# Performance work log

Hardware: AMD Instinct MI355X
Metric: run time of the kernel (lower is better)

## Reference

```python
import jax, jax.numpy as jnp
import numpy as np

N, E = 50000, 800000
NFEAT, NHID, NCLASS = 128, 64, 40
LN_EPS = 1e-5


def setup_inputs() -> dict:
    key = jax.random.key(0)
    ks = jax.random.split(key, 10)
    x = jax.random.normal(ks[0], (N, NFEAT), dtype=jnp.float32)
    edge_index = jax.random.randint(ks[1], (2, E), 0, N, dtype=jnp.int32)
    adj_vals = jax.random.uniform(ks[2], (E,), dtype=jnp.float32)
    s1 = 1.0 / NHID ** 0.5
    W1 = jax.random.uniform(ks[3], (NFEAT, NHID), minval=-s1, maxval=s1, dtype=jnp.float32)
    s2 = 1.0 / (2 * NHID) ** 0.5
    a1 = jax.random.uniform(ks[4], (2 * NHID, 1), minval=-s2, maxval=s2, dtype=jnp.float32)
    s3 = 1.0 / NCLASS ** 0.5
    W2 = jax.random.uniform(ks[5], (NHID, NCLASS), minval=-s3, maxval=s3, dtype=jnp.float32)
    # residual projection Linear(nfeat, nclass)
    sl = 1.0 / NFEAT ** 0.5
    res_w = jax.random.uniform(ks[6], (NCLASS, NFEAT), minval=-sl, maxval=sl, dtype=jnp.float32)
    res_b = jax.random.uniform(ks[7], (NCLASS,), minval=-sl, maxval=sl, dtype=jnp.float32)
    ln_g = jnp.ones((NCLASS,), dtype=jnp.float32)
    ln_b = jnp.zeros((NCLASS,), dtype=jnp.float32)
    return {"x": x, "edge_index": edge_index, "adj_vals": adj_vals,
            "W1": W1, "a1": a1, "W2": W2, "res_w": res_w, "res_b": res_b,
            "ln_g": ln_g, "ln_b": ln_b}


def reference(x, edge_index, adj_vals, W1, a1, W2, res_w, res_b, ln_g, ln_b):
    n = x.shape[0]
    row, col = edge_index[0], edge_index[1]
    h1 = x @ W1                                  # [N, nhid]
    # edge attention: cat([h1[row], h1[col]]) @ a1 == h1[row]@a_src + h1[col]@a_dst
    a_src, a_dst = a1[:NHID, 0], a1[NHID:, 0]
    scores = h1[row] @ a_src + h1[col] @ a_dst   # [E]
    scores = jax.nn.leaky_relu(scores, negative_slope=0.2)
    w = jax.nn.sigmoid(scores) * adj_vals        # [E] weighted adjacency values
    # sparse mm: out[row] += w * h[col]
    h1_out = jax.ops.segment_sum(w[:, None] * h1[col], row, num_segments=n)
    h1_out = jax.nn.relu(h1_out)
    h2 = h1_out @ W2                             # [N, nclass]
    h2_out = jax.ops.segment_sum(w[:, None] * h2[col], row, num_segments=n)
    h2_out = jax.nn.relu(h2_out)
    # residual projection + LayerNorm
    y = h2_out + (x @ res_w.T + res_b)
    mu = jnp.mean(y, axis=-1, keepdims=True)
    var = jnp.var(y, axis=-1, keepdims=True)
    y = (y - mu) * jax.lax.rsqrt(var + LN_EPS) * ln_g + ln_b
    return y
```

## Files before the change

### kernel.cpp

```cpp
#include <hip/hip_runtime.h>
#include <math.h>

#define N_NODES 50000
#define N_EDGES 800000
#define NFEAT 128
#define NHID 64
#define NCLASS 40
#define LN_EPS 1e-5f
#define BROWS 64
#define NBUCK ((N_NODES + BROWS - 1) / BROWS)
#define CHUNK 4096
#define NCHUNK ((N_EDGES + CHUNK - 1) / CHUNK)
#define NPB 16
#define H2ROWS 64

__device__ __forceinline__ int swz(int k) { return ((k >> 2) & 7) << 2; }

__device__ __forceinline__ unsigned packbf(float a, float b) {
  unsigned ua = __float_as_uint(a), ub = __float_as_uint(b);
  ua += 0x7fffu + ((ua >> 16) & 1u);
  ub += 0x7fffu + ((ub >> 16) & 1u);
  return (ua >> 16) | (ub & 0xffff0000u);
}
__device__ __forceinline__ unsigned bf16hi(float a) {
  unsigned u = __float_as_uint(a);
  u += 0x7fffu + ((u >> 16) & 1u);
  return u & 0xffff0000u;
}
__device__ __forceinline__ float lo16(unsigned v) { return __uint_as_float(v << 16); }
__device__ __forceinline__ float hi16(unsigned v) { return __uint_as_float(v & 0xffff0000u); }

__global__ __launch_bounds__(256) void k_h1mm(const float* __restrict__ x,
    const float* __restrict__ W1, const float* __restrict__ a1,
    unsigned* __restrict__ h1u, float* __restrict__ s_src, float* __restrict__ s_dst,
    int* __restrict__ bcnt) {
  __shared__ float xT[NFEAT * 64];
  __shared__ float W1s[NFEAT * NHID];
  int t = threadIdx.x;
  if (blockIdx.x == 0)
    for (int i = t; i < NBUCK; i += 256) bcnt[i] = 0;
  int R0 = blockIdx.x * 64;
  for (int i = t; i < NFEAT * NHID / 4; i += 256)
    ((float4*)W1s)[i] = ((const float4*)W1)[i];
#pragma unroll
  for (int it = 0; it < 8; ++it) {
    int i = t + it * 256;
    int r = i >> 5, kq = i & 31;
    int gr = R0 + r;
    float4 v = make_float4(0.f, 0.f, 0.f, 0.f);
    if (gr < N_NODES) v = *(const float4*)(x + (size_t)gr * NFEAT + kq * 4);
    int rw = r ^ ((kq & 7) << 2);
    xT[(kq * 4 + 0) * 64 + rw] = v.x;
    xT[(kq * 4 + 1) * 64 + rw] = v.y;
    xT[(kq * 4 + 2) * 64 + rw] = v.z;
    xT[(kq * 4 + 3) * 64 + rw] = v.w;
  }
  __syncthreads();
  int cg = t & 15, rg = t >> 4;
  int c0 = cg * 4, r0 = rg * 4;
  float acc[4][4] = {};
#pragma unroll 4
  for (int k = 0; k < NFEAT; ++k) {
    float4 xv = *(const float4*)&xT[k * 64 + (r0 ^ swz(k))];
    float4 wv = *(const float4*)&W1s[k * NHID + c0];
    float xr[4] = {xv.x, xv.y, xv.z, xv.w};
    float wr[4] = {wv.x, wv.y, wv.z, wv.w};
#pragma unroll
    for (int j = 0; j < 4; ++j)
#pragma unroll
      for (int c = 0; c < 4; ++c)
        acc[j][c] = fmaf(xr[j], wr[c], acc[j][c]);
  }
  float4 as = *(const float4*)(a1 + c0);
  float4 ad = *(const float4*)(a1 + NHID + c0);
  float asr[4] = {as.x, as.y, as.z, as.w};
  float adr[4] = {ad.x, ad.y, ad.z, ad.w};
  float ps[4], pd[4];
#pragma unroll
  for (int j = 0; j < 4; ++j) {
    int gr = R0 + r0 + j;
    if (gr < N_NODES) {
      uint2 pk;
      pk.x = packbf(acc[j][0], acc[j][1]);
      pk.y = packbf(acc[j][2], acc[j][3]);
      *(uint2*)&h1u[(size_t)gr * 32 + (c0 >> 1)] = pk;
    }
    float s = 0.f, d = 0.f;
#pragma unroll
    for (int c = 0; c < 4; ++c) {
      s = fmaf(acc[j][c], asr[c], s);
      d = fmaf(acc[j][c], adr[c], d);
    }
    ps[j] = s; pd[j] = d;
  }
#pragma unroll
  for (int j = 0; j < 4; ++j)
#pragma unroll
    for (int off = 1; off < 16; off <<= 1) {
      ps[j] += __shfl_xor(ps[j], off);
      pd[j] += __shfl_xor(pd[j], off);
    }
  if (cg == 0) {
#pragma unroll
    for (int j = 0; j < 4; ++j) {
      int gr = R0 + r0 + j;
      if (gr < N_NODES) { s_src[gr] = ps[j]; s_dst[gr] = pd[j]; }
    }
  }
}

__global__ __launch_bounds__(256) void k_resmm(const float* __restrict__ x,
    const float* __restrict__ res_w, const float* __restrict__ res_b,
    float* __restrict__ res) {
  __shared__ float xT[NFEAT * 128];
  __shared__ float rwT[NFEAT * NCLASS];
  int t = threadIdx.x;
  int R0 = blockIdx.x * 128;
  for (int i = t; i < NCLASS * NFEAT; i += 256) {
    int c = i / NFEAT, k = i % NFEAT;
    rwT[k * NCLASS + c] = res_w[i];
  }
#pragma unroll
  for (int it = 0; it < 16; ++it) {
    int i = t + it * 256;
    int r = i >> 5, kq = i & 31;
    int gr = R0 + r;
    float4 v = make_float4(0.f, 0.f, 0.f, 0.f);
    if (gr < N_NODES) v = *(const float4*)(x + (size_t)gr * NFEAT + kq * 4);
    int rw = r ^ ((kq & 7) << 2);
    xT[(kq * 4 + 0) * 128 + rw] = v.x;
    xT[(kq * 4 + 1) * 128 + rw] = v.y;
    xT[(kq * 4 + 2) * 128 + rw] = v.z;
    xT[(kq * 4 + 3) * 128 + rw] = v.w;
  }
  __syncthreads();
  int cg = t & 7, rg = t >> 3;
  int c0 = cg * 5, r0 = rg * 4;
  float acc[4][5] = {};
#pragma unroll 4
  for (int k = 0; k < NFEAT; ++k) {
    float4 xv = *(const float4*)&xT[k * 128 + (r0 ^ swz(k))];
    float xr[4] = {xv.x, xv.y, xv.z, xv.w};
    float wr[5];
#pragma unroll
    for (int c = 0; c < 5; ++c) wr[c] = rwT[k * NCLASS + c0 + c];
#pragma unroll
    for (int j = 0; j < 4; ++j)
#pragma unroll
      for (int c = 0; c < 5; ++c)
        acc[j][c] = fmaf(xr[j], wr[c], acc[j][c]);
  }
  float bb[5];
#pragma unroll
  for (int c = 0; c < 5; ++c) bb[c] = res_b[c0 + c];
#pragma unroll
  for (int j = 0; j < 4; ++j) {
    int gr = R0 + r0 + j;
    if (gr < N_NODES) {
#pragma unroll
      for (int c = 0; c < 5; ++c)
        res[(size_t)gr * NCLASS + c0 + c] = acc[j][c] + bb[c];
    }
  }
}

__global__ __launch_bounds__(256) void k_bhist(const int* __restrict__ ei,
    int* __restrict__ bcnt) {
  __shared__ int cnt[NBUCK];
  int t = threadIdx.x;
  int e0 = blockIdx.x * CHUNK;
  int ecnt = min(CHUNK, N_EDGES - e0);
  for (int i = t; i < NBUCK; i += 256) cnt[i] = 0;
  __syncthreads();
  for (int i = t; i < ecnt; i += 256)
    atomicAdd(&cnt[ei[e0 + i] >> 6], 1);
  __syncthreads();
  for (int i = t; i < NBUCK; i += 256)
    if (cnt[i]) atomicAdd(&bcnt[i], cnt[i]);
}

__global__ __launch_bounds__(256) void k_bscan(const int* __restrict__ bcnt,
    int* __restrict__ gptr, int* __restrict__ gfill) {
  __shared__ int psum[256];
  int t = threadIdx.x;
  int base = t * 4;
  int s[4];
#pragma unroll
  for (int j = 0; j < 4; ++j)
    s[j] = (base + j < NBUCK) ? bcnt[base + j] : 0;
  int local = s[0] + s[1] + s[2] + s[3];
  psum[t] = local;
  __syncthreads();
#pragma unroll
  for (int o = 1; o < 256; o <<= 1) {
    int v = (t >= o) ? psum[t - o] : 0;
    __syncthreads();
    psum[t] += v;
    __syncthreads();
  }
  int excl = psum[t] - local;
#pragma unroll
  for (int j = 0; j < 4; ++j) {
    if (base + j < NBUCK) gptr[base + j] = excl;
    excl += s[j];
  }
  if (t == 255) gptr[NBUCK] = psum[255];
  for (int i = t; i < NBUCK; i += 256) gfill[i] = 0;
}

__global__ __launch_bounds__(256) void k_bscatter(const int* __restrict__ ei,
    const float* __restrict__ adj, const int* __restrict__ gptr,
    int* __restrict__ gfill, uint2* __restrict__ edata) {
  __shared__ int cnt[NBUCK];
  __shared__ int off[NBUCK];
  __shared__ int gbase[NBUCK];
  __shared__ int po[NBUCK];
  __shared__ int psum[256];
  __shared__ uint2 stage[CHUNK];
  int t = threadIdx.x;
  int e0 = blockIdx.x * CHUNK;
  int ecnt = min(CHUNK, N_EDGES - e0);
  for (int i = t; i < NBUCK; i += 256) { cnt[i] = 0; po[i] = 0; }
  __syncthreads();
  for (int i = t; i < ecnt; i += 256)
    atomicAdd(&cnt[ei[e0 + i] >> 6], 1);
  __syncthreads();
  int base = t * 4;
  int s0 = (base < NBUCK) ? cnt[base] : 0;
  int s1 = (base + 1 < NBUCK) ? cnt[base + 1] : 0;
  int s2 = (base + 2 < NBUCK) ? cnt[base + 2] : 0;
  int s3 = (base + 3 < NBUCK) ? cnt[base + 3] : 0;
  int local = s0 + s1 + s2 + s3;
  psum[t] = local;
  __syncthreads();
#pragma unroll
  for (int o = 1; o < 256; o <<= 1) {
    int v = (t >= o) ? psum[t - o] : 0;
    __syncthreads();
    psum[t] += v;
    __syncthreads();
  }
  int excl = psum[t] - local;
  if (base < NBUCK) {
    off[base] = excl;
    if (s0 > 0) gbase[base] = gptr[base] + atomicAdd(&gfill[base], s0);
  }
  if (base + 1 < NBUCK) {
    off[base + 1] = excl + s0;
    if (s1 > 0) gbase[base + 1] = gptr[base + 1] + atomicAdd(&gfill[base + 1], s1);
  }
  if (base + 2 < NBUCK) {
    off[base + 2] = excl + s0 + s1;
    if (s2 > 0) gbase[base + 2] = gptr[base + 2] + atomicAdd(&gfill[base + 2], s2);
  }
  if (base + 3 < NBUCK) {
    off[base + 3] = excl + s0 + s1 + s2;
    if (s3 > 0) gbase[base + 3] = gptr[base + 3] + atomicAdd(&gfill[base + 3], s3);
  }
  __syncthreads();
  for (int i = t; i < ecnt; i += 256) {
    int e = e0 + i;
    int row = ei[e], col = ei[N_EDGES + e];
    int b = row >> 6;
    int pos = off[b] + atomicAdd(&po[b], 1);
    stage[pos] = make_uint2(((unsigned)b << 22) | ((unsigned)(row & 63) << 16) |
                            (unsigned)col, __float_as_uint(adj[e]));
  }
  __syncthreads();
  for (int i = t; i < ecnt; i += 256) {
    uint2 v = stage[i];
    int b = v.x >> 22;
    edata[(size_t)gbase[b] + (i - off[b])] = v;
  }
}

__global__ __launch_bounds__(256) void k_csr(const uint2* __restrict__ edata,
    const int* __restrict__ gptr, const float* __restrict__ s_src,
    const float* __restrict__ s_dst, int* __restrict__ row_ptr,
    unsigned* __restrict__ ecsr) {
  __shared__ int lcnt[BROWS];
  __shared__ int lexcl[BROWS];
  __shared__ int lfill[BROWS];
  __shared__ float ssrc[BROWS];
  int t = threadIdx.x;
  int b = blockIdx.x;
  int es = gptr[b], ee = gptr[b + 1];
  if (t < BROWS) {
    lcnt[t] = 0; lfill[t] = 0;
    int gn = b * BROWS + t;
    ssrc[t] = (gn < N_NODES) ? s_src[gn] : 0.f;
  }
  __syncthreads();
  for (int i = es + t; i < ee; i += 256)
    atomicAdd(&lcnt[(edata[i].x >> 16) & 63u], 1);
  __syncthreads();
  if (t < 64) {
    int v = lcnt[t];
    int sc = v;
#pragma unroll
    for (int o = 1; o < 64; o <<= 1) {
      int u = __shfl_up(sc, o);
      if (t >= o) sc += u;
    }
    lexcl[t] = sc - v;
    int gn = b * BROWS + t;
    if (gn < N_NODES) row_ptr[gn] = es + sc - v;
  }
  if (b == NBUCK - 1 && t == 0) row_ptr[N_NODES] = ee;
  __syncthreads();
  for (int i = es + t; i < ee; i += 256) {
    uint2 v = edata[i];
    int rl = (v.x >> 16) & 63;
    int col = v.x & 0xffffu;
    float sc = ssrc[rl] + s_dst[col];
    sc = (sc > 0.f) ? sc : 0.2f * sc;
    float wv = __uint_as_float(v.y) / (1.f + __expf(-sc));
    int pos = es + lexcl[rl] + atomicAdd(&lfill[rl], 1);
    ecsr[pos] = bf16hi(wv) | (unsigned)col;
  }
}

__global__ __launch_bounds__(256) void k_agg1(const unsigned* __restrict__ h1u,
    const unsigned* __restrict__ edata, const int* __restrict__ row_ptr,
    unsigned* __restrict__ h1o) {
  __shared__ int rps[NPB + 1];
  __shared__ float accs[NPB][NHID];
  int t = threadIdx.x;
  int n0 = blockIdx.x * NPB;
  if (t <= NPB) rps[t] = row_ptr[min(n0 + t, N_NODES)];
  for (int i = t; i < NPB * NHID / 4; i += 256)
    ((float4*)&accs[0][0])[i] = make_float4(0.f, 0.f, 0.f, 0.f);
  __syncthreads();
  int e0 = rps[0], e1 = rps[NPB];
  int span = e1 - e0;
  int gid = t >> 5, s = t & 31;
  int chunk = (span + 7) >> 3;
  int es = e0 + gid * chunk;
  int ee = min(es + chunk, e1);
  if (es < ee) {
    int lo = 0, hi = NPB - 1;
    while (lo < hi) { int mid = (lo + hi) >> 1; if (rps[mid + 1] <= es) lo = mid + 1; else hi = mid; }
    int r = lo, nxt = rps[r + 1];
    float acc0 = 0.f, acc1 = 0.f;
    int e = es;
    while (e < ee) {
      int m = ee - e; if (m > 8) m = 8;
      unsigned ue = (s < m) ? edata[e + s] : 0u;
      unsigned u[8], v[8];
#pragma unroll
      for (int i = 0; i < 8; ++i) u[i] = __shfl(ue, i, 32);
#pragma unroll
      for (int i = 0; i < 8; ++i) if (i < m) v[i] = h1u[(size_t)(u[i] & 0xffffu) * 32 + s];
#pragma unroll
      for (int i = 0; i < 8; ++i) if (i < m) {
        while (e + i >= nxt) {
          atomicAdd(&accs[r][2 * s], acc0);
          atomicAdd(&accs[r][2 * s + 1], acc1);
          acc0 = acc1 = 0.f; ++r; nxt = rps[r + 1];
        }
        float wv = hi16(u[i]);
        acc0 = fmaf(wv, lo16(v[i]), acc0);
        acc1 = fmaf(wv, hi16(v[i]), acc1);
      }
      e += m;
    }
    atomicAdd(&accs[r][2 * s], acc0);
    atomicAdd(&accs[r][2 * s + 1], acc1);
  }
  __syncthreads();
  for (int i = t; i < NPB * 32; i += 256) {
    int n = i >> 5, c = i & 31;
    int gn = n0 + n;
    if (gn < N_NODES)
      h1o[(size_t)gn * 32 + c] =
          packbf(fmaxf(accs[n][2 * c], 0.f), fmaxf(accs[n][2 * c + 1], 0.f));
  }
}

__global__ __launch_bounds__(256) void k_h2mm(const unsigned* __restrict__ h1o,
    const float* __restrict__ W2, unsigned short* __restrict__ h2s) {
  __shared__ unsigned xs[H2ROWS * 32];
  __shared__ float W2s[NHID * NCLASS];
  int t = threadIdx.x;
  int R0 = blockIdx.x * H2ROWS;
  for (int i = t; i < NHID * NCLASS; i += 256) W2s[i] = W2[i];
  for (int i = t; i < H2ROWS * 32; i += 256) {
    int r = i >> 5, ku = i & 31;
    int gr = R0 + r;
    unsigned v = (gr < N_NODES) ? h1o[(size_t)gr * 32 + ku] : 0u;
    xs[r * 32 + (ku ^ (r & 31))] = v;
  }
  __syncthreads();
  int q = t & 31, cg = t >> 5;
  int c0 = cg * 5;
  float acc[2][5] = {};
#pragma unroll 8
  for (int ku = 0; ku < 32; ++ku) {
    unsigned ua = xs[q * 32 + (ku ^ q)];
    unsigned ub = xs[(q + 32) * 32 + (ku ^ q)];
    float a0 = lo16(ua), a1 = hi16(ua);
    float b0 = lo16(ub), b1 = hi16(ub);
#pragma unroll
    for (int c = 0; c < 5; ++c) {
      float w0 = W2s[(2 * ku) * NCLASS + c0 + c];
      float w1 = W2s[(2 * ku + 1) * NCLASS + c0 + c];
      acc[0][c] = fmaf(a0, w0, acc[0][c]);
      acc[0][c] = fmaf(a1, w1, acc[0][c]);
      acc[1][c] = fmaf(b0, w0, acc[1][c]);
      acc[1][c] = fmaf(b1, w1, acc[1][c]);
    }
  }
#pragma unroll
  for (int j = 0; j < 2; ++j) {
    int gr = R0 + q + j * 32;
    if (gr < N_NODES) {
#pragma unroll
      for (int c = 0; c < 5; ++c)
        h2s[(size_t)gr * NCLASS + c0 + c] = (unsigned short)(bf16hi(acc[j][c]) >> 16);
    }
  }
}

__global__ __launch_bounds__(256) void k_agg2(const unsigned short* __restrict__ h2s,
    const unsigned* __restrict__ edata, const int* __restrict__ row_ptr,
    const float* __restrict__ res, const float* __restrict__ ln_g,
    const float* __restrict__ ln_b, float* __restrict__ out) {
  __shared__ int rps[NPB + 1];
  __shared__ float accs[NPB][NCLASS];
  int t = threadIdx.x;
  int n0 = blockIdx.x * NPB;
  if (t <= NPB) rps[t] = row_ptr[min(n0 + t, N_NODES)];
  for (int i = t; i < NPB * NCLASS; i += 256) ((float*)accs)[i] = 0.f;
  __syncthreads();
  int e0 = rps[0], e1 = rps[NPB];
  int span = e1 - e0;
  int gid = t >> 5, s = t & 31;
  int chunk = (span + 7) >> 3;
  int es = e0 + gid * chunk;
  int ee = min(es + chunk, e1);
  bool act = (s < 20);
  if (es < ee) {
    int lo = 0, hi = NPB - 1;
    while (lo < hi) { int mid = (lo + hi) >> 1; if (rps[mid + 1] <= es) lo = mid + 1; else hi = mid; }
    int r = lo, nxt = rps[r + 1];
    float acc0 = 0.f, acc1 = 0.f;
    int e = es;
    while (e < ee) {
      int m = ee - e; if (m > 8) m = 8;
      unsigned ue = (s < m) ? edata[e + s] : 0u;
      unsigned u[8], v[8];
#pragma unroll
      for (int i = 0; i < 8; ++i) u[i] = __shfl(ue, i, 32);
#pragma unroll
      for (int i = 0; i < 8; ++i) {
        v[i] = 0u;
        if (i < m && act)
          v[i] = *(const unsigned*)(h2s + (size_t)(u[i] & 0xffffu) * NCLASS + 2 * s);
      }
#pragma unroll
      for (int i = 0; i < 8; ++i) if (i < m) {
        while (e + i >= nxt) {
          if (act) {
            atomicAdd(&accs[r][2 * s], acc0);
            atomicAdd(&accs[r][2 * s + 1], acc1);
          }
          acc0 = acc1 = 0.f; ++r; nxt = rps[r + 1];
        }
        float wv = hi16(u[i]);
        acc0 = fmaf(wv, lo16(v[i]), acc0);
        acc1 = fmaf(wv, hi16(v[i]), acc1);
      }
      e += m;
    }
    if (act) {
      atomicAdd(&accs[r][2 * s], acc0);
      atomicAdd(&accs[r][2 * s + 1], acc1);
    }
  }
  __syncthreads();
  int wave = t >> 6, lane = t & 63;
  for (int k = 0; k < NPB / 4; ++k) {
    int n = wave * (NPB / 4) + k;
    int gn = n0 + n;
    if (gn >= N_NODES) break;
    float y = 0.f;
    if (lane < NCLASS)
      y = fmaxf(accs[n][lane], 0.f) + res[(size_t)gn * NCLASS + lane];
    float s1 = y, s2 = y * y;
#pragma unroll
    for (int off = 1; off < 64; off <<= 1) {
      s1 += __shfl_xor(s1, off);
      s2 += __shfl_xor(s2, off);
    }
    float mu = s1 / (float)NCLASS;
    float var = s2 / (float)NCLASS - mu * mu;
    float inv = rsqrtf(var + LN_EPS);
    if (lane < NCLASS)
      out[(size_t)gn * NCLASS + lane] = (y - mu) * inv * ln_g[lane] + ln_b[lane];
  }
}

extern "C" void kernel_launch(void* const* d_in, const int* in_sizes, int n_in,
                              void* d_out, int out_size, void* d_ws, size_t ws_size,
                              hipStream_t stream) {
  const float* x     = (const float*)d_in[0];
  const int*   ei    = (const int*)  d_in[1];
  const float* adj   = (const float*)d_in[2];
  const float* W1    = (const float*)d_in[3];
  const float* a1    = (const float*)d_in[4];
  const float* W2    = (const float*)d_in[5];
  const float* res_w = (const float*)d_in[6];
  const float* res_b = (const float*)d_in[7];
  const float* ln_g  = (const float*)d_in[8];
  const float* ln_b  = (const float*)d_in[9];
  float* out = (float*)d_out;

  char* ws = (char*)d_ws;
  size_t off = 0;
  auto alloc = [&](size_t bytes) -> void* {
    void* p = (void*)(ws + off);
    off += (bytes + 255) & ~(size_t)255;
    return p;
  };

  unsigned*       h1u     = (unsigned*)alloc((size_t)N_NODES * 32 * 4);
  float*          s_src   = (float*)alloc((size_t)N_NODES * 4);
  float*          s_dst   = (float*)alloc((size_t)N_NODES * 4);
  int*            bcnt    = (int*)alloc((size_t)NBUCK * 4);
  int*            gptr    = (int*)alloc((size_t)(NBUCK + 1) * 4);
  int*            gfill   = (int*)alloc((size_t)NBUCK * 4);
  int*            row_ptr = (int*)alloc((size_t)(N_NODES + 1) * 4);
  uint2*          edata   = (uint2*)alloc((size_t)N_EDGES * 8);
  unsigned*       ecsr    = (unsigned*)alloc((size_t)N_EDGES * 4);
  unsigned*       h1o     = (unsigned*)alloc((size_t)N_NODES * 32 * 4);
  unsigned short* h2s     = (unsigned short*)alloc((size_t)N_NODES * NCLASS * 2);
  float*          res     = (float*)alloc((size_t)N_NODES * NCLASS * 4);
  (void)ws_size; (void)in_sizes; (void)n_in; (void)out_size;

  const int NBLK_H1  = (N_NODES + 63) / 64;
  const int NBLK_RES = (N_NODES + 127) / 128;
  const int NBLK_H2  = (N_NODES + H2ROWS - 1) / H2ROWS;
  const int NBLK_AGG = (N_NODES + NPB - 1) / NPB;

  k_h1mm<<<NBLK_H1, 256, 0, stream>>>(x, W1, a1, h1u, s_src, s_dst, bcnt);
  k_resmm<<<NBLK_RES, 256, 0, stream>>>(x, res_w, res_b, res);
  k_bhist<<<NCHUNK, 256, 0, stream>>>(ei, bcnt);
  k_bscan<<<1, 256, 0, stream>>>(bcnt, gptr, gfill);
  k_bscatter<<<NCHUNK, 256, 0, stream>>>(ei, adj, gptr, gfill, edata);
  k_csr<<<NBUCK, 256, 0, stream>>>(edata, gptr, s_src, s_dst, row_ptr, ecsr);
  k_agg1<<<NBLK_AGG, 256, 0, stream>>>(h1u, ecsr, row_ptr, h1o);
  k_h2mm<<<NBLK_H2, 256, 0, stream>>>(h1o, W2, h2s);
  k_agg2<<<NBLK_AGG, 256, 0, stream>>>(h2s, ecsr, row_ptr, res, ln_g, ln_b, out);
}
```

Baseline: 191.7 us.

## Reorder second layer to aggregate h1 then apply W2 in agg2 epilogue

Uses linearity, (A·h1o)·W2 = A·(h1o·W2), to drop the separate h2 matmul kernel and its bf16 h2 buffer. The second aggregation now gathers 64-wide bf16 h1o rows (128 B) per edge instead of 40-wide h2 rows (80 B). Each block multiplies its 16 aggregated rows by W2, held in shared memory, before the LayerNorm epilogue. This saves one launch and an N×40 write and read, but raises gather traffic per edge and adds a W2 load per block. It also changes rounding, since h2 is no longer quantised to bf16.

```diff
diff --git a/kernel.cpp b/kernel.cpp
--- a/kernel.cpp
+++ b/kernel.cpp
@@ -12,7 +12,6 @@
 #define CHUNK 4096
 #define NCHUNK ((N_EDGES + CHUNK - 1) / CHUNK)
 #define NPB 16
-#define H2ROWS 64
 
 __device__ __forceinline__ int swz(int k) { return ((k >> 2) & 7) << 2; }
 
@@ -377,60 +376,20 @@
   }
 }
 
-__global__ __launch_bounds__(256) void k_h2mm(const unsigned* __restrict__ h1o,
-    const float* __restrict__ W2, unsigned short* __restrict__ h2s) {
-  __shared__ unsigned xs[H2ROWS * 32];
+__global__ __launch_bounds__(256) void k_agg2(const unsigned* __restrict__ h1o,
+    const unsigned* __restrict__ edata, const int* __restrict__ row_ptr,
+    const float* __restrict__ W2, const float* __restrict__ res,
+    const float* __restrict__ ln_g, const float* __restrict__ ln_b,
+    float* __restrict__ out) {
+  __shared__ int rps[NPB + 1];
+  __shared__ float accs[NPB][NHID];
   __shared__ float W2s[NHID * NCLASS];
-  int t = threadIdx.x;
-  int R0 = blockIdx.x * H2ROWS;
-  for (int i = t; i < NHID * NCLASS; i += 256) W2s[i] = W2[i];
-  for (int i = t; i < H2ROWS * 32; i += 256) {
-    int r = i >> 5, ku = i & 31;
-    int gr = R0 + r;
-    unsigned v = (gr < N_NODES) ? h1o[(size_t)gr * 32 + ku] : 0u;
-    xs[r * 32 + (ku ^ (r & 31))] = v;
-  }
-  __syncthreads();
-  int q = t & 31, cg = t >> 5;
-  int c0 = cg * 5;
-  float acc[2][5] = {};
-#pragma unroll 8
-  for (int ku = 0; ku < 32; ++ku) {
-    unsigned ua = xs[q * 32 + (ku ^ q)];
-    unsigned ub = xs[(q + 32) * 32 + (ku ^ q)];
-    float a0 = lo16(ua), a1 = hi16(ua);
-    float b0 = lo16(ub), b1 = hi16(ub);
-#pragma unroll
-    for (int c = 0; c < 5; ++c) {
-      float w0 = W2s[(2 * ku) * NCLASS + c0 + c];
-      float w1 = W2s[(2 * ku + 1) * NCLASS + c0 + c];
-      acc[0][c] = fmaf(a0, w0, acc[0][c]);
-      acc[0][c] = fmaf(a1, w1, acc[0][c]);
-      acc[1][c] = fmaf(b0, w0, acc[1][c]);
-      acc[1][c] = fmaf(b1, w1, acc[1][c]);
-    }
-  }
-#pragma unroll
-  for (int j = 0; j < 2; ++j) {
-    int gr = R0 + q + j * 32;
-    if (gr < N_NODES) {
-#pragma unroll
-      for (int c = 0; c < 5; ++c)
-        h2s[(size_t)gr * NCLASS + c0 + c] = (unsigned short)(bf16hi(acc[j][c]) >> 16);
-    }
-  }
-}
-
-__global__ __launch_bounds__(256) void k_agg2(const unsigned short* __restrict__ h2s,
-    const unsigned* __restrict__ edata, const int* __restrict__ row_ptr,
-    const float* __restrict__ res, const float* __restrict__ ln_g,
-    const float* __restrict__ ln_b, float* __restrict__ out) {
-  __shared__ int rps[NPB + 1];
-  __shared__ float accs[NPB][NCLASS];
   int t = threadIdx.x;
   int n0 = blockIdx.x * NPB;
   if (t <= NPB) rps[t] = row_ptr[min(n0 + t, N_NODES)];
-  for (int i = t; i < NPB * NCLASS; i += 256) ((float*)accs)[i] = 0.f;
+  for (int i = t; i < NHID * NCLASS; i += 256) W2s[i] = W2[i];
+  for (int i = t; i < NPB * NHID / 4; i += 256)
+    ((float4*)&accs[0][0])[i] = make_float4(0.f, 0.f, 0.f, 0.f);
   __syncthreads();
   int e0 = rps[0], e1 = rps[NPB];
   int span = e1 - e0;
@@ -438,7 +397,6 @@
   int chunk = (span + 7) >> 3;
   int es = e0 + gid * chunk;
   int ee = min(es + chunk, e1);
-  bool act = (s < 20);
   if (es < ee) {
     int lo = 0, hi = NPB - 1;
     while (lo < hi) { int mid = (lo + hi) >> 1; if (rps[mid + 1] <= es) lo = mid + 1; else hi = mid; }
@@ -452,18 +410,12 @@
 #pragma unroll
       for (int i = 0; i < 8; ++i) u[i] = __shfl(ue, i, 32);
 #pragma unroll
-      for (int i = 0; i < 8; ++i) {
-        v[i] = 0u;
-        if (i < m && act)
-          v[i] = *(const unsigned*)(h2s + (size_t)(u[i] & 0xffffu) * NCLASS + 2 * s);
-      }
+      for (int i = 0; i < 8; ++i) if (i < m) v[i] = h1o[(size_t)(u[i] & 0xffffu) * 32 + s];
 #pragma unroll
       for (int i = 0; i < 8; ++i) if (i < m) {
         while (e + i >= nxt) {
-          if (act) {
-            atomicAdd(&accs[r][2 * s], acc0);
-            atomicAdd(&accs[r][2 * s + 1], acc1);
-          }
+          atomicAdd(&accs[r][2 * s], acc0);
+          atomicAdd(&accs[r][2 * s + 1], acc1);
           acc0 = acc1 = 0.f; ++r; nxt = rps[r + 1];
         }
         float wv = hi16(u[i]);
@@ -472,10 +424,8 @@
       }
       e += m;
     }
-    if (act) {
-      atomicAdd(&accs[r][2 * s], acc0);
-      atomicAdd(&accs[r][2 * s + 1], acc1);
-    }
+    atomicAdd(&accs[r][2 * s], acc0);
+    atomicAdd(&accs[r][2 * s + 1], acc1);
   }
   __syncthreads();
   int wave = t >> 6, lane = t & 63;
@@ -484,8 +434,13 @@
     int gn = n0 + n;
     if (gn >= N_NODES) break;
     float y = 0.f;
-    if (lane < NCLASS)
-      y = fmaxf(accs[n][lane], 0.f) + res[(size_t)gn * NCLASS + lane];
+    if (lane < NCLASS) {
+      float sum = 0.f;
+#pragma unroll 8
+      for (int j = 0; j < NHID; ++j)
+        sum = fmaf(accs[n][j], W2s[j * NCLASS + lane], sum);
+      y = fmaxf(sum, 0.f) + res[(size_t)gn * NCLASS + lane];
+    }
     float s1 = y, s2 = y * y;
 #pragma unroll
     for (int off = 1; off < 64; off <<= 1) {
@@ -533,13 +488,11 @@
   uint2*          edata   = (uint2*)alloc((size_t)N_EDGES * 8);
   unsigned*       ecsr    = (unsigned*)alloc((size_t)N_EDGES * 4);
   unsigned*       h1o     = (unsigned*)alloc((size_t)N_NODES * 32 * 4);
-  unsigned short* h2s     = (unsigned short*)alloc((size_t)N_NODES * NCLASS * 2);
   float*          res     = (float*)alloc((size_t)N_NODES * NCLASS * 4);
   (void)ws_size; (void)in_sizes; (void)n_in; (void)out_size;
 
   const int NBLK_H1  = (N_NODES + 63) / 64;
   const int NBLK_RES = (N_NODES + 127) / 128;
-  const int NBLK_H2  = (N_NODES + H2ROWS - 1) / H2ROWS;
   const int NBLK_AGG = (N_NODES + NPB - 1) / NPB;
 
   k_h1mm<<<NBLK_H1, 256, 0, stream>>>(x, W1, a1, h1u, s_src, s_dst, bcnt);
@@ -549,6 +502,5 @@
   k_bscatter<<<NCHUNK, 256, 0, stream>>>(ei, adj, gptr, gfill, edata);
   k_csr<<<NBUCK, 256, 0, stream>>>(edata, gptr, s_src, s_dst, row_ptr, ecsr);
   k_agg1<<<NBLK_AGG, 256, 0, stream>>>(h1u, ecsr, row_ptr, h1o);
-  k_h2mm<<<NBLK_H2, 256, 0, stream>>>(h1o, W2, h2s);
-  k_agg2<<<NBLK_AGG, 256, 0, stream>>>(h2s, ecsr, row_ptr, res, ln_g, ln_b, out);
-}
+  k_agg2<<<NBLK_AGG, 256, 0, stream>>>(h1o, ecsr, row_ptr, W2, res, ln_g, ln_b, out);
+}
```

After: 204.9 us. +6.9%, slower.
